# Kernel optimization log

Hardware: AMD Instinct MI355X
Metric: run time of the kernel (lower is better)

## Reference

```python
import jax, jax.numpy as jnp
import numpy as np

N, IN_DIM, HEADS, OUT_DIM = 4096, 128, 4, 64
NEG_INF = -9.0e15  # finite mask value, matches torch source


def setup_inputs() -> dict:
    key = jax.random.key(0)
    k1, k2, k3, k4, k5 = jax.random.split(key, 5)
    x = jax.random.normal(k1, (N, IN_DIM), dtype=jnp.float32)
    adj_mask = jax.random.bernoulli(k2, 0.1, (N, N))  # bool, j->i edges
    # xavier-uniform-ish scales
    lim_w = float(np.sqrt(6.0 / (IN_DIM + HEADS * OUT_DIM)))
    W_lin = jax.random.uniform(k3, (IN_DIM, HEADS * OUT_DIM), minval=-lim_w, maxval=lim_w, dtype=jnp.float32)
    lim_a = float(np.sqrt(6.0 / (2 * OUT_DIM + 1)))
    a_src = jax.random.uniform(k4, (OUT_DIM,), minval=-lim_a, maxval=lim_a, dtype=jnp.float32)
    a_dst = jax.random.uniform(k5, (OUT_DIM,), minval=-lim_a, maxval=lim_a, dtype=jnp.float32)
    return {"x": x, "adj_mask": adj_mask, "W_lin": W_lin, "a_src": a_src, "a_dst": a_dst}


def reference(x, adj_mask, W_lin, a_src, a_dst):
    n = x.shape[0]
    h = (x @ W_lin).reshape(n, HEADS, OUT_DIM)           # (N, H, D)
    # att(cat(h_i, h_j)) decomposes linearly: a_src.h_i + a_dst.h_j
    s_i = jnp.einsum("nhd,d->nh", h, a_src)              # (N, H) contribution of dest node i
    s_j = jnp.einsum("nhd,d->nh", h, a_dst)              # (N, H) contribution of source node j
    e = jax.nn.leaky_relu(s_i[:, None, :] + s_j[None, :, :], 0.2)  # (N, N, H)
    e = jnp.where(adj_mask[:, :, None], e, NEG_INF)
    attn = jax.nn.softmax(e, axis=1)                     # softmax over source nodes j
    out = jnp.einsum("ijh,jhd->ihd", attn, h)            # per-head aggregation
    return out.reshape(n, HEADS * OUT_DIM)               # concat=True
```

## Files before the change

kernel.cpp:

```cpp
#include <hip/hip_runtime.h>
#include <math.h>


#define N 4096
#define IN_DIM 128
#define HEADS 4
#define OUT_DIM 64
#define HD 256
#define LOG2E 1.4426950408889634f
#define PSHIFT 8.0f

typedef _Float16 f16x8 __attribute__((ext_vector_type(8)));
typedef __fp16 fp16x2 __attribute__((ext_vector_type(2)));
typedef float f32x4 __attribute__((ext_vector_type(4)));

union F16x8u { fp16x2 h2[4]; f16x8 v; };

#define WS_HB_OFF    0u
#define WS_SSRC_OFF  2097152u
#define WS_SDT_OFF   2162688u
#define WS_BITT_OFF  2228224u
#define WS_HSUMP_OFF 4325376u
#define WS_PL_OFF    4849664u
#define WS_PART_OFF  5373952u
#define WS_NEED8     (5373952u + 8u * 4194304u)
#define WS_NEED2     (5373952u + 2u * 4194304u)

__device__ __forceinline__ float lrelu(float v) { return fmaxf(v, 0.2f * v); }

__device__ __forceinline__ unsigned pack_bytes(unsigned v) {
  return (v & 1u) | ((v >> 7) & 2u) | ((v >> 14) & 4u) | ((v >> 21) & 8u);
}

__global__ __launch_bounds__(256) void pack_mask_k(const void* __restrict__ mraw,
                                                   unsigned* __restrict__ bits_t) {
  __shared__ int s_flag;
  if (threadIdx.x == 0) s_flag = 0;
  __syncthreads();
  const unsigned* mw = (const unsigned*)mraw;
  int bad = 0, g = 0;
  for (int i = threadIdx.x; i < 1024; i += 256) {
    unsigned v = mw[i];
    if (v & 0xFEFEFEFEu) bad = 1;
    if (v > 1u) g = 1;
  }
  if (bad || g) atomicOr(&s_flag, (bad ? 1 : 0) | (g ? 2 : 0));
  __syncthreads();
  const bool byte_fmt = ((s_flag & 1) == 0) && ((s_flag & 2) != 0);

  int w = blockIdx.x * 256 + threadIdx.x;
  unsigned ob = 0u;
  if (byte_fmt) {
    const uint4* p = (const uint4*)((const unsigned char*)mraw + (size_t)w * 32u);
    uint4 a = p[0], b = p[1];
    ob  =  pack_bytes(a.x)        | (pack_bytes(a.y) << 4)  | (pack_bytes(a.z) << 8)  | (pack_bytes(a.w) << 12);
    ob |= (pack_bytes(b.x) << 16) | (pack_bytes(b.y) << 20) | (pack_bytes(b.z) << 24) | (pack_bytes(b.w) << 28);
  } else {
    const uint4* p = (const uint4*)((const unsigned*)mraw + (size_t)w * 32u);
#pragma unroll
    for (int k = 0; k < 8; ++k) {
      uint4 v = p[k];
      ob |= (v.x ? 1u : 0u) << (4 * k);
      ob |= (v.y ? 1u : 0u) << (4 * k + 1);
      ob |= (v.z ? 1u : 0u) << (4 * k + 2);
      ob |= (v.w ? 1u : 0u) << (4 * k + 3);
    }
  }
  const int row = w >> 7, jc = w & 127;
  bits_t[((size_t)(row >> 6) * 128 + jc) * 64 + (row & 63)] = ob;
}

__global__ __launch_bounds__(256) void compute_h(const float* __restrict__ x,
                                                 const float* __restrict__ W,
                                                 const float* __restrict__ a_src,
                                                 const float* __restrict__ a_dst,
                                                 _Float16* __restrict__ hb,
                                                 float* __restrict__ s_src,
                                                 float* __restrict__ s_dst_t,
                                                 float* __restrict__ hsum_part) {
  __shared__ float xs[8][IN_DIM];
  const int i0 = blockIdx.x * 8;
  const int c = threadIdx.x;

  ((float4*)&xs[0][0])[c] = ((const float4*)(x + (size_t)i0 * IN_DIM))[c];
  __syncthreads();

  float acc[8];
#pragma unroll
  for (int r = 0; r < 8; ++r) acc[r] = 0.f;

  for (int kk = 0; kk < IN_DIM / 4; ++kk) {
    const int k = kk * 4;
    float w0 = W[(size_t)(k + 0) * HD + c];
    float w1 = W[(size_t)(k + 1) * HD + c];
    float w2 = W[(size_t)(k + 2) * HD + c];
    float w3 = W[(size_t)(k + 3) * HD + c];
#pragma unroll
    for (int r = 0; r < 8; ++r) {
      float4 xv = *(const float4*)(&xs[r][k]);
      acc[r] = fmaf(xv.x, w0, fmaf(xv.y, w1, fmaf(xv.z, w2, fmaf(xv.w, w3, acc[r]))));
    }
  }

  {
    const int head = c >> 6, nt = (c >> 4) & 3, m15 = c & 15;
    const int unit = (head * 128 + (i0 >> 5)) * 4 + nt;
    const int lanep = ((i0 & 31) >> 3) * 16 + m15;
    f16x8 v;
#pragma unroll
    for (int r = 0; r < 8; ++r) v[r] = (_Float16)acc[r];
    *(f16x8*)(hb + (size_t)unit * 512 + lanep * 8) = v;
  }

  {
    float loc = 0.f;
#pragma unroll
    for (int r = 0; r < 8; ++r) loc += acc[r];
    hsum_part[(size_t)blockIdx.x * HD + c] = loc;
  }

  const int hw = c >> 6, lane = c & 63;
  const float as = a_src[lane], ad = a_dst[lane];
#pragma unroll
  for (int r = 0; r < 8; ++r) {
    float vs = acc[r] * as, vd = acc[r] * ad;
#pragma unroll
    for (int off = 1; off < 64; off <<= 1) {
      vs += __shfl_xor(vs, off);
      vd += __shfl_xor(vd, off);
    }
    if (lane == 0) {
      s_src[(size_t)(i0 + r) * HEADS + hw] = vs * LOG2E;
      s_dst_t[(size_t)hw * N + (i0 + r)] = vd * LOG2E;
    }
  }
}

__global__ __launch_bounds__(512, 4) void gat_aggr(const _Float16* __restrict__ hb,
                                                   const float* __restrict__ s_src,
                                                   const float* __restrict__ s_dst_t,
                                                   const unsigned* __restrict__ bits_t,
                                                   float* __restrict__ accp,
                                                   float* __restrict__ lp,
                                                   int jshift) {
  const int jsplit = 1 << jshift;
  const int jrange = N >> jshift;
  const int chunks = jrange >> 5;
  const int tid = threadIdx.x;
  const int wave = tid >> 6;
  const int lane = tid & 63;
  const int head = wave & 3;
  const int mg = wave >> 2;
  const int m15 = lane & 15;
  const int quad = lane >> 4;
  const int jq = blockIdx.x & (jsplit - 1);
  const int it = blockIdx.x >> jshift;
  const int i0 = it * 64;
  const int rA = i0 + mg * 32 + m15;
  const int rB = rA + 16;

  const float siA = s_src[(size_t)rA * HEADS + head];
  const float siB = s_src[(size_t)rB * HEADS + head];

  const unsigned* mt = bits_t + ((size_t)it * 128 + jq * chunks) * 64 + mg * 32 + m15;
  const float* sjb = s_dst_t + (size_t)head * N + jq * jrange + quad * 8;
  const _Float16* hbp = hb + ((size_t)(head * 128 + jq * chunks) * 4) * 512 + lane * 8;

  f32x4 accA0 = {0.f, 0.f, 0.f, 0.f}, accA1 = accA0, accA2 = accA0, accA3 = accA0;
  f32x4 accB0 = accA0, accB1 = accA0, accB2 = accA0, accB3 = accA0;
  float lA = 0.f, lB = 0.f;

  const int shq = quad * 8;

  for (int c = 0; c < chunks; ++c) {
    const unsigned mwA = mt[c * 64];
    const unsigned mwB = mt[c * 64 + 16];
    const float4 sa = *(const float4*)(sjb + c * 32);
    const float4 sb = *(const float4*)(sjb + c * 32 + 4);

    const f16x8 b0 = *(const f16x8*)(hbp + (size_t)(c * 4 + 0) * 512);
    const f16x8 b1 = *(const f16x8*)(hbp + (size_t)(c * 4 + 1) * 512);
    const f16x8 b2 = *(const f16x8*)(hbp + (size_t)(c * 4 + 2) * 512);
    const f16x8 b3 = *(const f16x8*)(hbp + (size_t)(c * 4 + 3) * 512);

    const unsigned wA = mwA >> shq;
    const unsigned wB = mwB >> shq;
    const float sjs[8] = {sa.x, sa.y, sa.z, sa.w, sb.x, sb.y, sb.z, sb.w};

    F16x8u uA, uB;
#pragma unroll
    for (int t2 = 0; t2 < 4; ++t2) {
      float pA[2], pB[2];
#pragma unroll
      for (int q = 0; q < 2; ++q) {
        const int t = t2 * 2 + q;
        const float sj = sjs[t];
        float vA = lrelu(siA + sj);
        float vB = lrelu(siB + sj);
        float xA = (((wA >> t) & 1u) ? vA : -1.0e38f) - PSHIFT;
        float xB = (((wB >> t) & 1u) ? vB : -1.0e38f) - PSHIFT;
        pA[q] = __builtin_amdgcn_exp2f(xA);
        pB[q] = __builtin_amdgcn_exp2f(xB);
        lA += pA[q];
        lB += pB[q];
      }
      uA.h2[t2] = __builtin_amdgcn_cvt_pkrtz(pA[0], pA[1]);
      uB.h2[t2] = __builtin_amdgcn_cvt_pkrtz(pB[0], pB[1]);
    }

    accA0 = __builtin_amdgcn_mfma_f32_16x16x32_f16(uA.v, b0, accA0, 0, 0, 0);
    accA1 = __builtin_amdgcn_mfma_f32_16x16x32_f16(uA.v, b1, accA1, 0, 0, 0);
    accA2 = __builtin_amdgcn_mfma_f32_16x16x32_f16(uA.v, b2, accA2, 0, 0, 0);
    accA3 = __builtin_amdgcn_mfma_f32_16x16x32_f16(uA.v, b3, accA3, 0, 0, 0);
    accB0 = __builtin_amdgcn_mfma_f32_16x16x32_f16(uB.v, b0, accB0, 0, 0, 0);
    accB1 = __builtin_amdgcn_mfma_f32_16x16x32_f16(uB.v, b1, accB1, 0, 0, 0);
    accB2 = __builtin_amdgcn_mfma_f32_16x16x32_f16(uB.v, b2, accB2, 0, 0, 0);
    accB3 = __builtin_amdgcn_mfma_f32_16x16x32_f16(uB.v, b3, accB3, 0, 0, 0);
  }

  lA += __shfl_xor(lA, 16); lA += __shfl_xor(lA, 32);
  lB += __shfl_xor(lB, 16); lB += __shfl_xor(lB, 32);
  if (quad == 0) {
    lp[((size_t)jq * N + rA) * HEADS + head] = lA;
    lp[((size_t)jq * N + rB) * HEADS + head] = lB;
  }

  const int colb = head * 64 + m15;
  float* oA = accp + (size_t)jq * (N * HD) + (size_t)(i0 + mg * 32 + quad * 4) * HD + colb;
  float* oB = oA + (size_t)16 * HD;
#pragma unroll
  for (int reg = 0; reg < 4; ++reg) {
    oA[(size_t)reg * HD + 0]  = accA0[reg];
    oA[(size_t)reg * HD + 16] = accA1[reg];
    oA[(size_t)reg * HD + 32] = accA2[reg];
    oA[(size_t)reg * HD + 48] = accA3[reg];
    oB[(size_t)reg * HD + 0]  = accB0[reg];
    oB[(size_t)reg * HD + 16] = accB1[reg];
    oB[(size_t)reg * HD + 32] = accB2[reg];
    oB[(size_t)reg * HD + 48] = accB3[reg];
  }
}

__global__ __launch_bounds__(256) void reduce_part(const float4* __restrict__ accp,
                                                   const float* __restrict__ lp,
                                                   const float* __restrict__ hsum_part,
                                                   float4* __restrict__ out, int jsplit) {
  const size_t idx = (size_t)blockIdx.x * 256 + threadIdx.x;
  const int row = (int)(idx >> 6);
  const int col4 = (int)(idx & 63);
  const int head = col4 >> 4;
  const size_t S = (size_t)N * HD / 4;

  float4 o = accp[idx];
  float lt = lp[(size_t)row * HEADS + head];
  for (int k = 1; k < jsplit; ++k) {
    float4 a = accp[idx + (size_t)k * S];
    o.x += a.x; o.y += a.y; o.z += a.z; o.w += a.w;
    lt += lp[((size_t)k * N + row) * HEADS + head];
  }
  if (lt == 0.f) {
    float4 hs = {0.f, 0.f, 0.f, 0.f};
    for (int b = 0; b < 512; ++b) {
      float4 t = ((const float4*)hsum_part)[(size_t)b * 64 + col4];
      hs.x += t.x; hs.y += t.y; hs.z += t.z; hs.w += t.w;
    }
    const float cst = 1.0f / (float)N;
    o.x = hs.x * cst; o.y = hs.y * cst; o.z = hs.z * cst; o.w = hs.w * cst;
  } else {
    const float inv = 1.0f / lt;
    o.x *= inv; o.y *= inv; o.z *= inv; o.w *= inv;
  }
  out[idx] = o;
}

extern "C" void kernel_launch(void* const* d_in, const int* in_sizes, int n_in,
                              void* d_out, int out_size, void* d_ws, size_t ws_size,
                              hipStream_t stream) {
  (void)in_sizes; (void)n_in; (void)out_size;
  const float* x = (const float*)d_in[0];
  const void* mask = d_in[1];
  const float* W = (const float*)d_in[2];
  const float* a_src = (const float*)d_in[3];
  const float* a_dst = (const float*)d_in[4];
  float* out = (float*)d_out;

  char* ws = (char*)d_ws;
  _Float16* hb = (_Float16*)(ws + WS_HB_OFF);
  float* s_src = (float*)(ws + WS_SSRC_OFF);
  float* s_dst_t = (float*)(ws + WS_SDT_OFF);
  unsigned* bits_t = (unsigned*)(ws + WS_BITT_OFF);
  float* hsum_part = (float*)(ws + WS_HSUMP_OFF);
  float* lp = (float*)(ws + WS_PL_OFF);
  float* accp = (float*)(ws + WS_PART_OFF);

  const int jshift = (ws_size >= (size_t)WS_NEED8) ? 3 : 1;
  const int jsplit = 1 << jshift;

  pack_mask_k<<<(N * N / 32) / 256, 256, 0, stream>>>(mask, bits_t);
  compute_h<<<N / 8, 256, 0, stream>>>(x, W, a_src, a_dst, hb, s_src, s_dst_t, hsum_part);
  gat_aggr<<<(N / 64) * jsplit, 512, 0, stream>>>(hb, s_src, s_dst_t, bits_t,
                                                  accp, lp, jshift);
  reduce_part<<<(N * HD / 4) / 256, 256, 0, stream>>>((const float4*)accp, lp, hsum_part,
                                                      (float4*)out, jsplit);
}
```

Before: 153.4 us.

## Fuse mask packing with projection and fold split-j reduction into aggregation

Merges the mask-packing and feature-projection kernels into one launch that dispatches by block index. It also removes the separate reduction kernel: each aggregation block bumps a per-row-tile atomic counter, and the last block to finish for that tile sums the partial accumulators and normalizers and writes the output. The aim is to cut launch count and inter-kernel gaps, at the cost of threadfence/atomic synchronisation and a serial tail reduction done by only one block per tile.

```diff
diff --git a/kernel.cpp b/kernel.cpp
--- a/kernel.cpp
+++ b/kernel.cpp
@@ -21,10 +21,11 @@
 #define WS_SDT_OFF   2162688u
 #define WS_BITT_OFF  2228224u
 #define WS_HSUMP_OFF 4325376u
-#define WS_PL_OFF    4849664u
-#define WS_PART_OFF  5373952u
-#define WS_NEED8     (5373952u + 8u * 4194304u)
-#define WS_NEED2     (5373952u + 2u * 4194304u)
+#define WS_CNT_OFF   4849664u
+#define WS_PL_OFF    4853760u
+#define WS_PART_OFF  5378048u
+#define WS_NEED8     (5378048u + 8u * 4194304u)
+#define WS_NEED2     (5378048u + 2u * 4194304u)
 
 __device__ __forceinline__ float lrelu(float v) { return fmaxf(v, 0.2f * v); }
 
@@ -32,106 +33,111 @@
   return (v & 1u) | ((v >> 7) & 2u) | ((v >> 14) & 4u) | ((v >> 21) & 8u);
 }
 
-__global__ __launch_bounds__(256) void pack_mask_k(const void* __restrict__ mraw,
-                                                   unsigned* __restrict__ bits_t) {
-  __shared__ int s_flag;
-  if (threadIdx.x == 0) s_flag = 0;
-  __syncthreads();
-  const unsigned* mw = (const unsigned*)mraw;
-  int bad = 0, g = 0;
-  for (int i = threadIdx.x; i < 1024; i += 256) {
-    unsigned v = mw[i];
-    if (v & 0xFEFEFEFEu) bad = 1;
-    if (v > 1u) g = 1;
-  }
-  if (bad || g) atomicOr(&s_flag, (bad ? 1 : 0) | (g ? 2 : 0));
-  __syncthreads();
-  const bool byte_fmt = ((s_flag & 1) == 0) && ((s_flag & 2) != 0);
-
-  int w = blockIdx.x * 256 + threadIdx.x;
-  unsigned ob = 0u;
-  if (byte_fmt) {
-    const uint4* p = (const uint4*)((const unsigned char*)mraw + (size_t)w * 32u);
-    uint4 a = p[0], b = p[1];
-    ob  =  pack_bytes(a.x)        | (pack_bytes(a.y) << 4)  | (pack_bytes(a.z) << 8)  | (pack_bytes(a.w) << 12);
-    ob |= (pack_bytes(b.x) << 16) | (pack_bytes(b.y) << 20) | (pack_bytes(b.z) << 24) | (pack_bytes(b.w) << 28);
+__global__ __launch_bounds__(256) void prep_k(const void* __restrict__ mraw,
+                                              unsigned* __restrict__ bits_t,
+                                              const float* __restrict__ x,
+                                              const float* __restrict__ W,
+                                              const float* __restrict__ a_src,
+                                              const float* __restrict__ a_dst,
+                                              _Float16* __restrict__ hb,
+                                              float* __restrict__ s_src,
+                                              float* __restrict__ s_dst_t,
+                                              float* __restrict__ hsum_part,
+                                              unsigned* __restrict__ cnt) {
+  if (blockIdx.x < 2048) {
+    if (blockIdx.x < 64 && threadIdx.x == 0) cnt[blockIdx.x] = 0u;
+
+    __shared__ int s_flag;
+    if (threadIdx.x == 0) s_flag = 0;
+    __syncthreads();
+    const unsigned* mw = (const unsigned*)mraw;
+    int bad = 0, g = 0;
+    for (int i = threadIdx.x; i < 1024; i += 256) {
+      unsigned v = mw[i];
+      if (v & 0xFEFEFEFEu) bad = 1;
+      if (v > 1u) g = 1;
+    }
+    if (bad || g) atomicOr(&s_flag, (bad ? 1 : 0) | (g ? 2 : 0));
+    __syncthreads();
+    const bool byte_fmt = ((s_flag & 1) == 0) && ((s_flag & 2) != 0);
+
+    int w = blockIdx.x * 256 + threadIdx.x;
+    unsigned ob = 0u;
+    if (byte_fmt) {
+      const uint4* p = (const uint4*)((const unsigned char*)mraw + (size_t)w * 32u);
+      uint4 a = p[0], b = p[1];
+      ob  =  pack_bytes(a.x)        | (pack_bytes(a.y) << 4)  | (pack_bytes(a.z) << 8)  | (pack_bytes(a.w) << 12);
+      ob |= (pack_bytes(b.x) << 16) | (pack_bytes(b.y) << 20) | (pack_bytes(b.z) << 24) | (pack_bytes(b.w) << 28);
+    } else {
+      const uint4* p = (const uint4*)((const unsigned*)mraw + (size_t)w * 32u);
+#pragma unroll
+      for (int k = 0; k < 8; ++k) {
+        uint4 v = p[k];
+        ob |= (v.x ? 1u : 0u) << (4 * k);
+        ob |= (v.y ? 1u : 0u) << (4 * k + 1);
+        ob |= (v.z ? 1u : 0u) << (4 * k + 2);
+        ob |= (v.w ? 1u : 0u) << (4 * k + 3);
+      }
+    }
+    const int row = w >> 7, jc = w & 127;
+    bits_t[((size_t)(row >> 6) * 128 + jc) * 64 + (row & 63)] = ob;
   } else {
-    const uint4* p = (const uint4*)((const unsigned*)mraw + (size_t)w * 32u);
-#pragma unroll
-    for (int k = 0; k < 8; ++k) {
-      uint4 v = p[k];
-      ob |= (v.x ? 1u : 0u) << (4 * k);
-      ob |= (v.y ? 1u : 0u) << (4 * k + 1);
-      ob |= (v.z ? 1u : 0u) << (4 * k + 2);
-      ob |= (v.w ? 1u : 0u) << (4 * k + 3);
-    }
-  }
-  const int row = w >> 7, jc = w & 127;
-  bits_t[((size_t)(row >> 6) * 128 + jc) * 64 + (row & 63)] = ob;
-}
-
-__global__ __launch_bounds__(256) void compute_h(const float* __restrict__ x,
-                                                 const float* __restrict__ W,
-                                                 const float* __restrict__ a_src,
-                                                 const float* __restrict__ a_dst,
-                                                 _Float16* __restrict__ hb,
-                                                 float* __restrict__ s_src,
-                                                 float* __restrict__ s_dst_t,
-                                                 float* __restrict__ hsum_part) {
-  __shared__ float xs[8][IN_DIM];
-  const int i0 = blockIdx.x * 8;
-  const int c = threadIdx.x;
-
-  ((float4*)&xs[0][0])[c] = ((const float4*)(x + (size_t)i0 * IN_DIM))[c];
-  __syncthreads();
-
-  float acc[8];
-#pragma unroll
-  for (int r = 0; r < 8; ++r) acc[r] = 0.f;
-
-  for (int kk = 0; kk < IN_DIM / 4; ++kk) {
-    const int k = kk * 4;
-    float w0 = W[(size_t)(k + 0) * HD + c];
-    float w1 = W[(size_t)(k + 1) * HD + c];
-    float w2 = W[(size_t)(k + 2) * HD + c];
-    float w3 = W[(size_t)(k + 3) * HD + c];
+    __shared__ float xs[8][IN_DIM];
+    const int blk = blockIdx.x - 2048;
+    const int i0 = blk * 8;
+    const int c = threadIdx.x;
+
+    ((float4*)&xs[0][0])[c] = ((const float4*)(x + (size_t)i0 * IN_DIM))[c];
+    __syncthreads();
+
+    float acc[8];
+#pragma unroll
+    for (int r = 0; r < 8; ++r) acc[r] = 0.f;
+
+    for (int kk = 0; kk < IN_DIM / 4; ++kk) {
+      const int k = kk * 4;
+      float w0 = W[(size_t)(k + 0) * HD + c];
+      float w1 = W[(size_t)(k + 1) * HD + c];
+      float w2 = W[(size_t)(k + 2) * HD + c];
+      float w3 = W[(size_t)(k + 3) * HD + c];
+#pragma unroll
+      for (int r = 0; r < 8; ++r) {
+        float4 xv = *(const float4*)(&xs[r][k]);
+        acc[r] = fmaf(xv.x, w0, fmaf(xv.y, w1, fmaf(xv.z, w2, fmaf(xv.w, w3, acc[r]))));
+      }
+    }
+
+    {
+      const int head = c >> 6, nt = (c >> 4) & 3, m15 = c & 15;
+      const int unit = (head * 128 + (i0 >> 5)) * 4 + nt;
+      const int lanep = ((i0 & 31) >> 3) * 16 + m15;
+      f16x8 v;
+#pragma unroll
+      for (int r = 0; r < 8; ++r) v[r] = (_Float16)acc[r];
+      *(f16x8*)(hb + (size_t)unit * 512 + lanep * 8) = v;
+    }
+
+    {
+      float loc = 0.f;
+#pragma unroll
+      for (int r = 0; r < 8; ++r) loc += acc[r];
+      hsum_part[(size_t)blk * HD + c] = loc;
+    }
+
+    const int hw = c >> 6, lane = c & 63;
+    const float as = a_src[lane], ad = a_dst[lane];
 #pragma unroll
     for (int r = 0; r < 8; ++r) {
-      float4 xv = *(const float4*)(&xs[r][k]);
-      acc[r] = fmaf(xv.x, w0, fmaf(xv.y, w1, fmaf(xv.z, w2, fmaf(xv.w, w3, acc[r]))));
-    }
-  }
-
-  {
-    const int head = c >> 6, nt = (c >> 4) & 3, m15 = c & 15;
-    const int unit = (head * 128 + (i0 >> 5)) * 4 + nt;
-    const int lanep = ((i0 & 31) >> 3) * 16 + m15;
-    f16x8 v;
-#pragma unroll
-    for (int r = 0; r < 8; ++r) v[r] = (_Float16)acc[r];
-    *(f16x8*)(hb + (size_t)unit * 512 + lanep * 8) = v;
-  }
-
-  {
-    float loc = 0.f;
-#pragma unroll
-    for (int r = 0; r < 8; ++r) loc += acc[r];
-    hsum_part[(size_t)blockIdx.x * HD + c] = loc;
-  }
-
-  const int hw = c >> 6, lane = c & 63;
-  const float as = a_src[lane], ad = a_dst[lane];
-#pragma unroll
-  for (int r = 0; r < 8; ++r) {
-    float vs = acc[r] * as, vd = acc[r] * ad;
-#pragma unroll
-    for (int off = 1; off < 64; off <<= 1) {
-      vs += __shfl_xor(vs, off);
-      vd += __shfl_xor(vd, off);
-    }
-    if (lane == 0) {
-      s_src[(size_t)(i0 + r) * HEADS + hw] = vs * LOG2E;
-      s_dst_t[(size_t)hw * N + (i0 + r)] = vd * LOG2E;
+      float vs = acc[r] * as, vd = acc[r] * ad;
+#pragma unroll
+      for (int off = 1; off < 64; off <<= 1) {
+        vs += __shfl_xor(vs, off);
+        vd += __shfl_xor(vd, off);
+      }
+      if (lane == 0) {
+        s_src[(size_t)(i0 + r) * HEADS + hw] = vs * LOG2E;
+        s_dst_t[(size_t)hw * N + (i0 + r)] = vd * LOG2E;
+      }
     }
   }
 }
@@ -142,7 +148,11 @@
                                                    const unsigned* __restrict__ bits_t,
                                                    float* __restrict__ accp,
                                                    float* __restrict__ lp,
+                                                   const float* __restrict__ hsum_part,
+                                                   unsigned* __restrict__ cnt,
+                                                   float* __restrict__ out,
                                                    int jshift) {
+  __shared__ unsigned s_old;
   const int jsplit = 1 << jshift;
   const int jrange = N >> jshift;
   const int chunks = jrange >> 5;
@@ -239,38 +249,43 @@
     oB[(size_t)reg * HD + 32] = accB2[reg];
     oB[(size_t)reg * HD + 48] = accB3[reg];
   }
-}
-
-__global__ __launch_bounds__(256) void reduce_part(const float4* __restrict__ accp,
-                                                   const float* __restrict__ lp,
-                                                   const float* __restrict__ hsum_part,
-                                                   float4* __restrict__ out, int jsplit) {
-  const size_t idx = (size_t)blockIdx.x * 256 + threadIdx.x;
-  const int row = (int)(idx >> 6);
-  const int col4 = (int)(idx & 63);
-  const int head = col4 >> 4;
-  const size_t S = (size_t)N * HD / 4;
-
-  float4 o = accp[idx];
-  float lt = lp[(size_t)row * HEADS + head];
-  for (int k = 1; k < jsplit; ++k) {
-    float4 a = accp[idx + (size_t)k * S];
-    o.x += a.x; o.y += a.y; o.z += a.z; o.w += a.w;
-    lt += lp[((size_t)k * N + row) * HEADS + head];
-  }
-  if (lt == 0.f) {
-    float4 hs = {0.f, 0.f, 0.f, 0.f};
-    for (int b = 0; b < 512; ++b) {
-      float4 t = ((const float4*)hsum_part)[(size_t)b * 64 + col4];
-      hs.x += t.x; hs.y += t.y; hs.z += t.z; hs.w += t.w;
-    }
-    const float cst = 1.0f / (float)N;
-    o.x = hs.x * cst; o.y = hs.y * cst; o.z = hs.z * cst; o.w = hs.w * cst;
-  } else {
-    const float inv = 1.0f / lt;
-    o.x *= inv; o.y *= inv; o.z *= inv; o.w *= inv;
-  }
-  out[idx] = o;
+
+  __syncthreads();
+  if (tid == 0) {
+    __threadfence();
+    s_old = atomicAdd(&cnt[it], 1u);
+  }
+  __syncthreads();
+  if (s_old == (unsigned)(jsplit - 1)) {
+    __threadfence();
+    const size_t S = (size_t)N * HD;
+    for (int e = tid; e < 64 * 64; e += 512) {
+      const int r = e >> 6;
+      const int c4 = e & 63;
+      const int row = i0 + r;
+      const int hd = c4 >> 4;
+      float4 o = {0.f, 0.f, 0.f, 0.f};
+      float lt = 0.f;
+      for (int k = 0; k < jsplit; ++k) {
+        float4 a = *((const float4*)(accp + (size_t)k * S) + (size_t)row * 64 + c4);
+        o.x += a.x; o.y += a.y; o.z += a.z; o.w += a.w;
+        lt += lp[((size_t)k * N + row) * HEADS + hd];
+      }
+      if (lt == 0.f) {
+        float4 hs = {0.f, 0.f, 0.f, 0.f};
+        for (int b = 0; b < 512; ++b) {
+          float4 t = ((const float4*)hsum_part)[(size_t)b * 64 + c4];
+          hs.x += t.x; hs.y += t.y; hs.z += t.z; hs.w += t.w;
+        }
+        const float cst = 1.0f / (float)N;
+        o.x = hs.x * cst; o.y = hs.y * cst; o.z = hs.z * cst; o.w = hs.w * cst;
+      } else {
+        const float inv = 1.0f / lt;
+        o.x *= inv; o.y *= inv; o.z *= inv; o.w *= inv;
+      }
+      ((float4*)out)[(size_t)row * 64 + c4] = o;
+    }
+  }
 }
 
 extern "C" void kernel_launch(void* const* d_in, const int* in_sizes, int n_in,
@@ -290,16 +305,15 @@
   float* s_dst_t = (float*)(ws + WS_SDT_OFF);
   unsigned* bits_t = (unsigned*)(ws + WS_BITT_OFF);
   float* hsum_part = (float*)(ws + WS_HSUMP_OFF);
+  unsigned* cnt = (unsigned*)(ws + WS_CNT_OFF);
   float* lp = (float*)(ws + WS_PL_OFF);
   float* accp = (float*)(ws + WS_PART_OFF);
 
   const int jshift = (ws_size >= (size_t)WS_NEED8) ? 3 : 1;
   const int jsplit = 1 << jshift;
 
-  pack_mask_k<<<(N * N / 32) / 256, 256, 0, stream>>>(mask, bits_t);
-  compute_h<<<N / 8, 256, 0, stream>>>(x, W, a_src, a_dst, hb, s_src, s_dst_t, hsum_part);
+  prep_k<<<2048 + N / 8, 256, 0, stream>>>(mask, bits_t, x, W, a_src, a_dst,
+                                           hb, s_src, s_dst_t, hsum_part, cnt);
   gat_aggr<<<(N / 64) * jsplit, 512, 0, stream>>>(hb, s_src, s_dst_t, bits_t,
-                                                  accp, lp, jshift);
-  reduce_part<<<(N * HD / 4) / 256, 256, 0, stream>>>((const float4*)accp, lp, hsum_part,
-                                                      (float4*)out, jsplit);
+                                                  accp, lp, hsum_part, cnt, out, jshift);
 }
```

Measured after the change: 240.6 us. 56.8% more time.
